# Kernel tuning notes

Hardware: AMD Instinct MI355X
Metric: run time of the kernel (lower is better)

The kernel has to match this reference:

```python
import jax, jax.numpy as jnp
import numpy as np

HIDDEN = 2048
NUM_EXPERTS = 8
TOP_K = 2
CAPACITY_FACTOR = 1.5
B, S = 2, 2048


def setup_inputs() -> dict:
    key = jax.random.key(0)
    k0, k1, k2 = jax.random.split(key, 3)
    hidden_states = jax.random.normal(k0, (B, S, HIDDEN), dtype=jnp.float32)
    # xavier-normal init per nn.init.xavier_normal_
    std1 = float(np.sqrt(2.0 / (HIDDEN + HIDDEN)))
    std2 = float(np.sqrt(2.0 / (HIDDEN + NUM_EXPERTS)))
    w1 = jax.random.normal(k1, (HIDDEN, HIDDEN), dtype=jnp.float32) * std1
    b1 = jnp.zeros((HIDDEN,), dtype=jnp.float32)
    w2 = jax.random.normal(k2, (NUM_EXPERTS, HIDDEN), dtype=jnp.float32) * std2
    b2 = jnp.zeros((NUM_EXPERTS,), dtype=jnp.float32)
    return {"hidden_states": hidden_states, "w1": w1, "b1": b1, "w2": w2, "b2": b2}


def reference(hidden_states, w1, b1, w2, b2):
    Bs, Ss, H = hidden_states.shape
    E, K = NUM_EXPERTS, TOP_K
    T = Bs * Ss
    capacity = int(T * CAPACITY_FACTOR * K / E)

    # router MLP: Linear -> ReLU -> Linear (dropout=0 -> identity)
    h = jax.nn.relu(jnp.einsum('bsh,oh->bso', hidden_states, w1) + b1)
    router_logits = jnp.einsum('bsh,eh->bse', h, w2) + b2  # [B,S,E]
    router_probs = jax.nn.softmax(router_logits, axis=-1)

    top_k_probs, top_k_indices = jax.lax.top_k(router_probs, K)  # [B,S,K]
    top_k_probs = top_k_probs / (jnp.sum(top_k_probs, axis=-1, keepdims=True) + 1e-8)

    # dispatch/combine: tokens claim capacity slots in (b,s,k) order.
    fe = top_k_indices.reshape(-1)            # [T*K] expert id per assignment
    fp = top_k_probs.reshape(-1)              # [T*K] prob per assignment
    onehot = (fe[:, None] == jnp.arange(E)[None, :]).astype(jnp.int32)  # [T*K,E]
    cum = jnp.cumsum(onehot, axis=0)          # running per-expert counts
    pos = jnp.take_along_axis(cum, fe[:, None], axis=1)[:, 0] - 1        # slot index
    valid = pos < capacity
    pos_c = jnp.minimum(pos, capacity - 1)
    tok = jnp.arange(T * K) // K              # flat token index

    dispatch = jnp.zeros((T, E, capacity), dtype=router_probs.dtype)
    combine = jnp.zeros((T, E, capacity), dtype=router_probs.dtype)
    dispatch = dispatch.at[tok, fe, pos_c].add(valid.astype(router_probs.dtype))
    combine = combine.at[tok, fe, pos_c].add(jnp.where(valid, fp, 0.0))
    dispatch_tensor = dispatch.reshape(Bs, Ss, E, capacity)
    combine_tensor = combine.reshape(Bs, Ss, E, capacity)

    # load-balancing aux loss
    router_prob_per_expert = jnp.mean(router_probs, axis=(0, 1))          # [E]
    expert_mask = jax.nn.one_hot(top_k_indices, E, dtype=router_probs.dtype)  # [B,S,K,E]
    expert_usage_rate = jnp.mean(expert_mask, axis=(0, 1, 2))             # [E]
    aux_loss = jnp.sum(router_prob_per_expert * expert_usage_rate) * E

    return dispatch_tensor, combine_tensor, router_probs, aux_loss
```

## Files before the change

kernel.cpp:

```cpp
#include <hip/hip_runtime.h>

#define HID   2048
#define NE    8
#define NK    2
#define NTOK  4096
#define NASS  (NTOK * NK)
#define CAP   1536
#define DISP_ELEMS ((size_t)NTOK * NE * CAP)
#define KBLK  (HID / 32)

typedef __bf16 bf16x8 __attribute__((ext_vector_type(8)));
typedef float  f32x4  __attribute__((ext_vector_type(4)));

typedef const __attribute__((address_space(1))) unsigned int GUint;
typedef       __attribute__((address_space(3))) unsigned int LUint;

__device__ __forceinline__ void gload16(const void* g, void* l) {
    __builtin_amdgcn_global_load_lds((GUint*)g, (LUint*)l, 16, 0, 0);
}

__global__ __launch_bounds__(256) void split_kernel(
    const float* __restrict__ src, __bf16* __restrict__ dst, int nblk)
{
    int g = blockIdx.x * 256 + threadIdx.x;
    if (g >= nblk * 4) return;
    int blk = g >> 2, sub = g & 3;
    const float* s = src + (size_t)blk * 32 + sub * 8;
    float x[8];
    float4 v0 = ((const float4*)s)[0], v1 = ((const float4*)s)[1];
    x[0]=v0.x; x[1]=v0.y; x[2]=v0.z; x[3]=v0.w;
    x[4]=v1.x; x[5]=v1.y; x[6]=v1.z; x[7]=v1.w;
    bf16x8 h8, l8;
#pragma unroll
    for (int j = 0; j < 8; ++j) {
        __bf16 h = (__bf16)x[j];
        h8[j] = h;
        l8[j] = (__bf16)(x[j] - (float)h);
    }
    __bf16* d = dst + (size_t)blk * 64;
    *(bf16x8*)(d + sub * 8)      = h8;
    *(bf16x8*)(d + 32 + sub * 8) = l8;
}

__global__ __launch_bounds__(256, 2) void gemm1_mfma_kernel(
    const __bf16* __restrict__ Xs,
    const __bf16* __restrict__ Ws,
    const float* __restrict__ b1, float* __restrict__ hout)
{
    __shared__ __bf16 As[2][128 * 64];
    __shared__ __bf16 Bs[2][128 * 64];

    const int tid  = threadIdx.x;
    const int wid  = tid >> 6;
    const int lane = tid & 63;

    int wg  = blockIdx.x;
    int swz = (wg & 7) * 64 + (wg >> 3);
    const int bx = swz & 15;
    const int by = swz >> 4;
    const int brow = by * 128;
    const int bcol = bx * 128;

    const int srow   = lane >> 3;
    const int sslot  = lane & 7;

    const int wr = wid >> 1, wc = wid & 1;
    const int fr = lane & 15;
    const int fc = lane >> 4;

    f32x4 acc[4][4];
#pragma unroll
    for (int m = 0; m < 4; ++m)
#pragma unroll
        for (int n = 0; n < 4; ++n) acc[m][n] = (f32x4)0.f;

#define STAGE(buf, b)                                                          \
    {                                                                          \
        _Pragma("unroll")                                                      \
        for (int i = 0; i < 4; ++i) {                                          \
            int ra = wid * 32 + i * 8 + srow;                                  \
            int ca = sslot ^ (ra & 7);                                         \
            gload16(Xs + ((size_t)(brow + ra) * KBLK + (b)) * 64 + ca * 8,     \
                    &As[buf][(wid * 32 + i * 8) * 64]);                        \
            int rb = wid * 32 + i * 8 + srow;                                  \
            int cb = sslot ^ (rb & 7);                                         \
            gload16(Ws + ((size_t)(bcol + rb) * KBLK + (b)) * 64 + cb * 8,     \
                    &Bs[buf][(wid * 32 + i * 8) * 64]);                        \
        }                                                                      \
    }

    int cur = 0;
    STAGE(0, 0);
    __syncthreads();

    for (int b = 0; b < KBLK; ++b) {
        if (b + 1 < KBLK) STAGE(cur ^ 1, b + 1);

        bf16x8 ah[4], al[4], bh[4], bl[4];
#pragma unroll
        for (int m = 0; m < 4; ++m) {
            int ra = wr * 64 + m * 16 + fr;
            ah[m] = *(const bf16x8*)&As[cur][ra * 64 + ((fc       ^ (ra & 7)) << 3)];
            al[m] = *(const bf16x8*)&As[cur][ra * 64 + (((4 + fc) ^ (ra & 7)) << 3)];
        }
#pragma unroll
        for (int n = 0; n < 4; ++n) {
            int rb = wc * 64 + n * 16 + fr;
            bh[n] = *(const bf16x8*)&Bs[cur][rb * 64 + ((fc       ^ (rb & 7)) << 3)];
            bl[n] = *(const bf16x8*)&Bs[cur][rb * 64 + (((4 + fc) ^ (rb & 7)) << 3)];
        }

#pragma unroll
        for (int m = 0; m < 4; ++m)
#pragma unroll
            for (int n = 0; n < 4; ++n) {
                f32x4 c = acc[m][n];
                c = __builtin_amdgcn_mfma_f32_16x16x32_bf16(ah[m], bh[n], c, 0, 0, 0);
                c = __builtin_amdgcn_mfma_f32_16x16x32_bf16(al[m], bh[n], c, 0, 0, 0);
                c = __builtin_amdgcn_mfma_f32_16x16x32_bf16(ah[m], bl[n], c, 0, 0, 0);
                acc[m][n] = c;
            }

        __syncthreads();
        cur ^= 1;
    }

#pragma unroll
    for (int m = 0; m < 4; ++m) {
#pragma unroll
        for (int n = 0; n < 4; ++n) {
            int row = brow + wr * 64 + m * 16 + fc * 4;
            int col = bcol + wc * 64 + n * 16 + fr;
            float bias = b1[col];
#pragma unroll
            for (int j = 0; j < 4; ++j) {
                float v = acc[m][n][j] + bias;
                hout[(size_t)(row + j) * HID + col] = fmaxf(v, 0.f);
            }
        }
    }
#undef STAGE
}

__global__ __launch_bounds__(256) void router_kernel(
    const float* __restrict__ hbuf, const float* __restrict__ w2,
    const float* __restrict__ b2, float* __restrict__ probs_out,
    int* __restrict__ topk_e, float* __restrict__ topk_p)
{
    const int t    = (blockIdx.x * 256 + threadIdx.x) >> 6;
    const int lane = threadIdx.x & 63;
    const float* hrow = hbuf + (size_t)t * HID;

    float acc[NE];
#pragma unroll
    for (int e = 0; e < NE; ++e) acc[e] = 0.f;

#pragma unroll
    for (int j = 0; j < HID / (64 * 4); ++j) {
        const int o = (j * 64 + lane) * 4;
        float4 hv = *(const float4*)(hrow + o);
#pragma unroll
        for (int e = 0; e < NE; ++e) {
            float4 wv = *(const float4*)(w2 + e * HID + o);
            acc[e] += hv.x * wv.x + hv.y * wv.y + hv.z * wv.z + hv.w * wv.w;
        }
    }
#pragma unroll
    for (int m = 32; m > 0; m >>= 1)
#pragma unroll
        for (int e = 0; e < NE; ++e) acc[e] += __shfl_xor(acc[e], m);

    if (lane == 0) {
        float lg[NE];
        float mx = -1e30f;
#pragma unroll
        for (int e = 0; e < NE; ++e) { lg[e] = acc[e] + b2[e]; mx = fmaxf(mx, lg[e]); }
        float sum = 0.f;
#pragma unroll
        for (int e = 0; e < NE; ++e) { lg[e] = expf(lg[e] - mx); sum += lg[e]; }
        float inv = 1.f / sum;
        float p[NE];
#pragma unroll
        for (int e = 0; e < NE; ++e) { p[e] = lg[e] * inv; probs_out[t * NE + e] = p[e]; }
        int e1 = 0;
#pragma unroll
        for (int e = 1; e < NE; ++e) if (p[e] > p[e1]) e1 = e;
        int e2 = -1;
#pragma unroll
        for (int e = 0; e < NE; ++e) if (e != e1 && (e2 < 0 || p[e] > p[e2])) e2 = e;
        float denom = p[e1] + p[e2] + 1e-8f;
        topk_e[t * NK + 0] = e1;
        topk_e[t * NK + 1] = e2;
        topk_p[t * NK + 0] = p[e1] / denom;
        topk_p[t * NK + 1] = p[e2] / denom;
    }
}

__global__ __launch_bounds__(256) void positions_kernel(
    const int* __restrict__ topk_e, int* __restrict__ pos)
{
    const int tid = threadIdx.x;
    __shared__ int sc[256][NE];
    int cnt[NE];
#pragma unroll
    for (int e = 0; e < NE; ++e) cnt[e] = 0;
    const int base = tid * 32;
    for (int i = 0; i < 32; ++i) cnt[topk_e[base + i]]++;
#pragma unroll
    for (int e = 0; e < NE; ++e) sc[tid][e] = cnt[e];
    __syncthreads();
    if (tid < NE) {
        int run = 0;
        for (int i = 0; i < 256; ++i) { int v = sc[i][tid]; sc[i][tid] = run; run += v; }
    }
    __syncthreads();
    int run[NE];
#pragma unroll
    for (int e = 0; e < NE; ++e) run[e] = sc[tid][e];
    for (int i = 0; i < 32; ++i) {
        int e = topk_e[base + i];
        pos[base + i] = run[e]++;
    }
}

__global__ __launch_bounds__(256) void zerofill_kernel(float* __restrict__ dst)
{
    const size_t n4 = 2 * DISP_ELEMS / 4;
    const size_t stride = (size_t)gridDim.x * 256;
    f32x4 z = (f32x4)0.f;
    f32x4* __restrict__ d = (f32x4*)dst;
    for (size_t i = blockIdx.x * 256 + threadIdx.x; i < n4; i += stride)
        __builtin_nontemporal_store(z, d + i);
}

__global__ __launch_bounds__(256) void scatter_kernel(
    const int* __restrict__ topk_e, const float* __restrict__ topk_p,
    const int* __restrict__ pos, float* __restrict__ dispatch,
    float* __restrict__ combine)
{
    const int a = blockIdx.x * 256 + threadIdx.x;
    if (a >= NASS) return;
    const int p = pos[a];
    if (p < CAP) {
        const int t = a >> 1;
        const int e = topk_e[a];
        const size_t off = ((size_t)t * NE + e) * CAP + p;
        dispatch[off] = 1.0f;
        combine[off]  = topk_p[a];
    }
}

__global__ __launch_bounds__(256) void aux_kernel(
    const float* __restrict__ probs, const int* __restrict__ topk_e,
    float* __restrict__ aux_out)
{
    const int tid = threadIdx.x;
    float ps[NE];
    int   cs[NE];
#pragma unroll
    for (int e = 0; e < NE; ++e) { ps[e] = 0.f; cs[e] = 0; }
    for (int t = tid; t < NTOK; t += 256)
#pragma unroll
        for (int e = 0; e < NE; ++e) ps[e] += probs[t * NE + e];
    for (int a = tid; a < NASS; a += 256) cs[topk_e[a]]++;

    __shared__ float rps[256][NE];
    __shared__ int   rcs[256][NE];
#pragma unroll
    for (int e = 0; e < NE; ++e) { rps[tid][e] = ps[e]; rcs[tid][e] = cs[e]; }
    __syncthreads();
    for (int s = 128; s > 0; s >>= 1) {
        if (tid < s) {
#pragma unroll
            for (int e = 0; e < NE; ++e) {
                rps[tid][e] += rps[tid + s][e];
                rcs[tid][e] += rcs[tid + s][e];
            }
        }
        __syncthreads();
    }
    if (tid == 0) {
        float aux = 0.f;
#pragma unroll
        for (int e = 0; e < NE; ++e)
            aux += (rps[0][e] / (float)NTOK) * ((float)rcs[0][e] / (float)NASS);
        aux_out[0] = aux * (float)NE;
    }
}

extern "C" void kernel_launch(void* const* d_in, const int* in_sizes, int n_in,
                              void* d_out, int out_size, void* d_ws, size_t ws_size,
                              hipStream_t stream)
{
    const float* X  = (const float*)d_in[0];
    const float* w1 = (const float*)d_in[1];
    const float* b1 = (const float*)d_in[2];
    const float* w2 = (const float*)d_in[3];
    const float* b2 = (const float*)d_in[4];

    float* out      = (float*)d_out;
    float* dispatch = out;
    float* combine  = out + DISP_ELEMS;
    float* probs    = out + 2 * DISP_ELEMS;
    float* aux      = out + 2 * DISP_ELEMS + (size_t)NTOK * NE;

    float*  hbuf = dispatch;
    __bf16* Xs   = (__bf16*)(dispatch + (size_t)NTOK * HID);
    __bf16* Ws   = Xs + (size_t)NTOK * HID * 2;

    int*   topk_e = (int*)d_ws;
    int*   pos    = (int*)d_ws + NASS;
    float* topk_p = (float*)((int*)d_ws + 2 * NASS);

    split_kernel<<<(NTOK * KBLK * 4 + 255) / 256, 256, 0, stream>>>(X,  Xs, NTOK * KBLK);
    split_kernel<<<(HID  * KBLK * 4 + 255) / 256, 256, 0, stream>>>(w1, Ws, HID * KBLK);
    gemm1_mfma_kernel<<<512, 256, 0, stream>>>(Xs, Ws, b1, hbuf);
    router_kernel<<<NTOK / 4, 256, 0, stream>>>(hbuf, w2, b2, probs, topk_e, topk_p);
    positions_kernel<<<1, 256, 0, stream>>>(topk_e, pos);
    zerofill_kernel<<<2048, 256, 0, stream>>>(out);
    scatter_kernel<<<(NASS + 255) / 256, 256, 0, stream>>>(topk_e, topk_p, pos, dispatch, combine);
    aux_kernel<<<1, 256, 0, stream>>>(probs, topk_e, aux);
}
```

Before: 585.2 us.

## Fold dispatch/combine zero-fill into GEMM loop and fuse tail kernels

Removes the standalone zero-fill kernel over the dispatch and combine outputs. Each GEMM workgroup now issues three nontemporal zero stores per K iteration, so the large memset overlaps with MFMA compute. Because the GEMM scratch (hbuf, split X/W) can no longer live inside the dispatch region, it moves into the workspace. The positions, scatter and aux-loss kernels are merged into one single-block finalize kernel that reuses per-expert totals for the usage rate. The extra store traffic may compete with the GEMM's operand loads, and the design relies on the workspace being large enough for the relocated buffers.

```diff
diff --git a/kernel.cpp b/kernel.cpp
--- a/kernel.cpp
+++ b/kernel.cpp
@@ -8,6 +8,7 @@
 #define CAP   1536
 #define DISP_ELEMS ((size_t)NTOK * NE * CAP)
 #define KBLK  (HID / 32)
+#define ZCHUNKS_PER_BLK 49152
 
 typedef __bf16 bf16x8 __attribute__((ext_vector_type(8)));
 typedef float  f32x4  __attribute__((ext_vector_type(4)));
@@ -45,7 +46,8 @@
 __global__ __launch_bounds__(256, 2) void gemm1_mfma_kernel(
     const __bf16* __restrict__ Xs,
     const __bf16* __restrict__ Ws,
-    const float* __restrict__ b1, float* __restrict__ hout)
+    const float* __restrict__ b1, float* __restrict__ hout,
+    float* __restrict__ zout)
 {
     __shared__ __bf16 As[2][128 * 64];
     __shared__ __bf16 Bs[2][128 * 64];
@@ -67,6 +69,9 @@
     const int wr = wid >> 1, wc = wid & 1;
     const int fr = lane & 15;
     const int fc = lane >> 4;
+
+    f32x4* zdst = (f32x4*)zout + (size_t)blockIdx.x * ZCHUNKS_PER_BLK + tid;
+    const f32x4 zz = (f32x4)0.f;
 
     f32x4 acc[4][4];
 #pragma unroll
@@ -96,6 +101,13 @@
     for (int b = 0; b < KBLK; ++b) {
         if (b + 1 < KBLK) STAGE(cur ^ 1, b + 1);
 
+        {
+            f32x4* z = zdst + (size_t)b * 768;
+            __builtin_nontemporal_store(zz, z);
+            __builtin_nontemporal_store(zz, z + 256);
+            __builtin_nontemporal_store(zz, z + 512);
+        }
+
         bf16x8 ah[4], al[4], bh[4], bl[4];
 #pragma unroll
         for (int m = 0; m < 4; ++m) {
@@ -196,86 +208,59 @@
     }
 }
 
-__global__ __launch_bounds__(256) void positions_kernel(
-    const int* __restrict__ topk_e, int* __restrict__ pos)
+__global__ __launch_bounds__(256) void finalize_kernel(
+    const int* __restrict__ topk_e, const float* __restrict__ topk_p,
+    const float* __restrict__ probs, float* __restrict__ dispatch,
+    float* __restrict__ combine, float* __restrict__ aux_out)
 {
     const int tid = threadIdx.x;
-    __shared__ int sc[256][NE];
+    __shared__ int   sc[256][NE];
+    __shared__ float tot[NE];
+    __shared__ float rps[256][NE];
+
     int cnt[NE];
 #pragma unroll
     for (int e = 0; e < NE; ++e) cnt[e] = 0;
     const int base = tid * 32;
-    for (int i = 0; i < 32; ++i) cnt[topk_e[base + i]]++;
+    int eloc[32];
+    for (int i = 0; i < 32; ++i) { eloc[i] = topk_e[base + i]; cnt[eloc[i]]++; }
 #pragma unroll
     for (int e = 0; e < NE; ++e) sc[tid][e] = cnt[e];
     __syncthreads();
     if (tid < NE) {
         int run = 0;
         for (int i = 0; i < 256; ++i) { int v = sc[i][tid]; sc[i][tid] = run; run += v; }
+        tot[tid] = (float)run;
     }
     __syncthreads();
     int run[NE];
 #pragma unroll
     for (int e = 0; e < NE; ++e) run[e] = sc[tid][e];
     for (int i = 0; i < 32; ++i) {
-        int e = topk_e[base + i];
-        pos[base + i] = run[e]++;
-    }
-}
-
-__global__ __launch_bounds__(256) void zerofill_kernel(float* __restrict__ dst)
-{
-    const size_t n4 = 2 * DISP_ELEMS / 4;
-    const size_t stride = (size_t)gridDim.x * 256;
-    f32x4 z = (f32x4)0.f;
-    f32x4* __restrict__ d = (f32x4*)dst;
-    for (size_t i = blockIdx.x * 256 + threadIdx.x; i < n4; i += stride)
-        __builtin_nontemporal_store(z, d + i);
-}
-
-__global__ __launch_bounds__(256) void scatter_kernel(
-    const int* __restrict__ topk_e, const float* __restrict__ topk_p,
-    const int* __restrict__ pos, float* __restrict__ dispatch,
-    float* __restrict__ combine)
-{
-    const int a = blockIdx.x * 256 + threadIdx.x;
-    if (a >= NASS) return;
-    const int p = pos[a];
-    if (p < CAP) {
-        const int t = a >> 1;
-        const int e = topk_e[a];
-        const size_t off = ((size_t)t * NE + e) * CAP + p;
-        dispatch[off] = 1.0f;
-        combine[off]  = topk_p[a];
-    }
-}
-
-__global__ __launch_bounds__(256) void aux_kernel(
-    const float* __restrict__ probs, const int* __restrict__ topk_e,
-    float* __restrict__ aux_out)
-{
-    const int tid = threadIdx.x;
+        const int a = base + i;
+        const int e = eloc[i];
+        const int p = run[e]++;
+        if (p < CAP) {
+            const int t = a >> 1;
+            const size_t off = ((size_t)t * NE + e) * CAP + p;
+            dispatch[off] = 1.0f;
+            combine[off]  = topk_p[a];
+        }
+    }
+
     float ps[NE];
-    int   cs[NE];
-#pragma unroll
-    for (int e = 0; e < NE; ++e) { ps[e] = 0.f; cs[e] = 0; }
+#pragma unroll
+    for (int e = 0; e < NE; ++e) ps[e] = 0.f;
     for (int t = tid; t < NTOK; t += 256)
 #pragma unroll
         for (int e = 0; e < NE; ++e) ps[e] += probs[t * NE + e];
-    for (int a = tid; a < NASS; a += 256) cs[topk_e[a]]++;
-
-    __shared__ float rps[256][NE];
-    __shared__ int   rcs[256][NE];
-#pragma unroll
-    for (int e = 0; e < NE; ++e) { rps[tid][e] = ps[e]; rcs[tid][e] = cs[e]; }
+#pragma unroll
+    for (int e = 0; e < NE; ++e) rps[tid][e] = ps[e];
     __syncthreads();
     for (int s = 128; s > 0; s >>= 1) {
         if (tid < s) {
 #pragma unroll
-            for (int e = 0; e < NE; ++e) {
-                rps[tid][e] += rps[tid + s][e];
-                rcs[tid][e] += rcs[tid + s][e];
-            }
+            for (int e = 0; e < NE; ++e) rps[tid][e] += rps[tid + s][e];
         }
         __syncthreads();
     }
@@ -283,7 +268,7 @@
         float aux = 0.f;
 #pragma unroll
         for (int e = 0; e < NE; ++e)
-            aux += (rps[0][e] / (float)NTOK) * ((float)rcs[0][e] / (float)NASS);
+            aux += (rps[0][e] / (float)NTOK) * (tot[e] / (float)NASS);
         aux_out[0] = aux * (float)NE;
     }
 }
@@ -304,20 +289,15 @@
     float* probs    = out + 2 * DISP_ELEMS;
     float* aux      = out + 2 * DISP_ELEMS + (size_t)NTOK * NE;
 
-    float*  hbuf = dispatch;
-    __bf16* Xs   = (__bf16*)(dispatch + (size_t)NTOK * HID);
-    __bf16* Ws   = Xs + (size_t)NTOK * HID * 2;
-
-    int*   topk_e = (int*)d_ws;
-    int*   pos    = (int*)d_ws + NASS;
-    float* topk_p = (float*)((int*)d_ws + 2 * NASS);
+    __bf16* Xs     = (__bf16*)d_ws;
+    __bf16* Ws     = Xs + (size_t)NTOK * HID * 2;
+    float*  hbuf   = (float*)(Ws + (size_t)HID * HID * 2);
+    int*    topk_e = (int*)(hbuf + (size_t)NTOK * HID);
+    float*  topk_p = (float*)(topk_e + NASS);
 
     split_kernel<<<(NTOK * KBLK * 4 + 255) / 256, 256, 0, stream>>>(X,  Xs, NTOK * KBLK);
     split_kernel<<<(HID  * KBLK * 4 + 255) / 256, 256, 0, stream>>>(w1, Ws, HID * KBLK);
-    gemm1_mfma_kernel<<<512, 256, 0, stream>>>(Xs, Ws, b1, hbuf);
+    gemm1_mfma_kernel<<<512, 256, 0, stream>>>(Xs, Ws, b1, hbuf, out);
     router_kernel<<<NTOK / 4, 256, 0, stream>>>(hbuf, w2, b2, probs, topk_e, topk_p);
-    positions_kernel<<<1, 256, 0, stream>>>(topk_e, pos);
-    zerofill_kernel<<<2048, 256, 0, stream>>>(out);
-    scatter_kernel<<<(NASS + 255) / 256, 256, 0, stream>>>(topk_e, topk_p, pos, dispatch, combine);
-    aux_kernel<<<1, 256, 0, stream>>>(probs, topk_e, aux);
-}
+    finalize_kernel<<<1, 256, 0, stream>>>(topk_e, topk_p, probs, dispatch, combine, aux);
+}
```

Result: faster. 506.0 us (-13.5%).
